# Kernel tuning notes

Measured on AMD Instinct MI355X. Metric: run time of the kernel, lower is better.

Reference implementation:

```python
import jax, jax.numpy as jnp
import numpy as np

B, T, D, H = 64, 1024, 256, 256

def setup_inputs() -> dict:
    key = jax.random.key(0)
    k1, k2, k3 = jax.random.split(key, 3)
    s = 1.0 / np.sqrt(H)
    return {
        "x": jax.random.normal(k1, (B, T, D), dtype=jnp.float32),
        "W_ih": jax.random.uniform(k2, (H, D), dtype=jnp.float32, minval=-s, maxval=s),
        "W_hh": jax.random.uniform(k3, (H, H), dtype=jnp.float32, minval=-s, maxval=s),
        "b_ih": jnp.zeros((H,), dtype=jnp.float32),
        "b_hh": jnp.zeros((H,), dtype=jnp.float32),
    }

def reference(x, W_ih, W_hh, b_ih, b_hh):
    # Precompute input projections for all timesteps at once (same math,
    # avoids T small GEMMs): [B, T, H]
    x_proj = jnp.einsum("btd,hd->bth", x, W_ih) + b_ih
    h0 = jnp.zeros((x.shape[0], W_hh.shape[0]), dtype=x.dtype)

    def step(h, xp_t):
        h_new = jnp.tanh(xp_t + h @ W_hh.T + b_hh)
        return h_new, h_new  # output of vanilla RNN cell is the new hidden state

    # scan over time: xp time-major [T, B, H]
    _, outs = jax.lax.scan(step, h0, jnp.swapaxes(x_proj, 0, 1))
    return jnp.swapaxes(outs, 0, 1)  # [B, T, H]
```

## Files before the change

### kernel.cpp

```cpp
#include <hip/hip_runtime.h>

#define BB 64
#define TT 1024
#define DD 256
#define HH 256
#define CH 8
#define NCH (TT / CH)

typedef float vf4 __attribute__((ext_vector_type(4)));
typedef float vf2 __attribute__((ext_vector_type(2)));
struct alignas(16) v2x2 { vf2 lo, hi; };

#define LD4(p) (*(const vf4*)(p))
#define LD2(p) (*(const vf2*)(p))
#define LDW(p) (*(const v2x2*)(p))

__device__ __forceinline__ float fast_tanh(float x) {
    float e = __expf(2.0f * x);
    return 1.0f - 2.0f / (e + 1.0f);
}

#define PKFMA(acc, aa, bb) acc = __builtin_elementwise_fma((aa), (bb), (acc))

#define DPPADD(dst, src, CTRL) {                                                   \
    int _di = __builtin_amdgcn_update_dpp(0, __float_as_int(src), CTRL, 0xF, 0xF, true); \
    dst = (src) + __int_as_float(_di); }

#define FMR(rr, bb, ss)                   \
    rr.x = fmaf((ss), (bb).x, rr.x);      \
    rr.y = fmaf((ss), (bb).y, rr.y);      \
    rr.z = fmaf((ss), (bb).z, rr.z);      \
    rr.w = fmaf((ss), (bb).w, rr.w)

#define BKb 32
#define LDP 132

__global__ __attribute__((amdgpu_flat_work_group_size(256, 256),
                          amdgpu_waves_per_eu(4, 4)))
void xproj_kernel(const float* __restrict__ x, const float* __restrict__ W_ih,
                  const float* __restrict__ b_ih, float* __restrict__ xp)
{
    __shared__ float As[BKb][LDP];
    __shared__ float Bs[BKb][LDP];

    const int tid = threadIdx.x;
    const int nb = blockIdx.x & 1;
    const int mb = blockIdx.x >> 1;
    const int m0 = mb * 128;
    const int n0 = nb * 128;

    const int sr = tid >> 3;
    const int sk = (tid & 7) * 4;

    const int tx = tid & 15;
    const int ty = tid >> 4;
    const int ma = ty * 4, mh = 64 + ty * 4;
    const int na = tx * 4, nh = 64 + tx * 4;

    vf4 ra0 = 0, ra1 = 0, ra2 = 0, ra3 = 0, ra4 = 0, ra5 = 0, ra6 = 0, ra7 = 0;
    vf4 rb0 = 0, rb1 = 0, rb2 = 0, rb3 = 0, rb4 = 0, rb5 = 0, rb6 = 0, rb7 = 0;

    for (int k0 = 0; k0 < DD; k0 += BKb) {
        #pragma unroll
        for (int g = 0; g < 4; ++g) {
            const int r = sr + g * 32;
            const vf4 v = LD4(x + (size_t)(m0 + r) * DD + k0 + sk);
            As[sk + 0][r] = v.x; As[sk + 1][r] = v.y;
            As[sk + 2][r] = v.z; As[sk + 3][r] = v.w;
        }
        #pragma unroll
        for (int g = 0; g < 4; ++g) {
            const int n = sr + g * 32;
            const vf4 v = LD4(W_ih + (size_t)(n0 + n) * DD + k0 + sk);
            Bs[sk + 0][n] = v.x; Bs[sk + 1][n] = v.y;
            Bs[sk + 2][n] = v.z; Bs[sk + 3][n] = v.w;
        }
        __syncthreads();

        #pragma unroll
        for (int kk = 0; kk < BKb; ++kk) {
            const vf4 alo = LD4(&As[kk][ma]);
            const vf4 ahi = LD4(&As[kk][mh]);
            const vf4 bl  = LD4(&Bs[kk][na]);
            const vf4 bh  = LD4(&Bs[kk][nh]);
            FMR(ra0, bl, alo.x); FMR(rb0, bh, alo.x);
            FMR(ra1, bl, alo.y); FMR(rb1, bh, alo.y);
            FMR(ra2, bl, alo.z); FMR(rb2, bh, alo.z);
            FMR(ra3, bl, alo.w); FMR(rb3, bh, alo.w);
            FMR(ra4, bl, ahi.x); FMR(rb4, bh, ahi.x);
            FMR(ra5, bl, ahi.y); FMR(rb5, bh, ahi.y);
            FMR(ra6, bl, ahi.z); FMR(rb6, bh, ahi.z);
            FMR(ra7, bl, ahi.w); FMR(rb7, bh, ahi.w);
        }
        __syncthreads();
    }

    const vf4 bia = LD4(b_ih + n0 + na);
    const vf4 bib = LD4(b_ih + n0 + nh);

    #define STORE_ROW(m, rA, rB)                                   \
        {                                                          \
            float* outp = xp + (size_t)(m0 + (m)) * HH + n0;       \
            *(vf4*)(outp + na) = rA + bia;                         \
            *(vf4*)(outp + nh) = rB + bib;                         \
        }
    STORE_ROW(ma + 0, ra0, rb0); STORE_ROW(ma + 1, ra1, rb1);
    STORE_ROW(ma + 2, ra2, rb2); STORE_ROW(ma + 3, ra3, rb3);
    STORE_ROW(mh + 0, ra4, rb4); STORE_ROW(mh + 1, ra5, rb5);
    STORE_ROW(mh + 2, ra6, rb6); STORE_ROW(mh + 3, ra7, rb7);
    #undef STORE_ROW
}

__global__ __attribute__((amdgpu_flat_work_group_size(1024, 1024),
                          amdgpu_waves_per_eu(4, 4)))
void rnn_kernel(const float* __restrict__ W_hh, const float* __restrict__ b_hh,
                const float* __restrict__ xpin, float* __restrict__ hout)
{
    const int tid = threadIdx.x;
    const int jg = tid >> 4;
    const int c  = tid & 15;
    const int j0 = jg * 4;
    const int jmine = j0 + (c & 3);
    const int b = blockIdx.x;

    __shared__ float hbuf[2][16 * 20];
    __shared__ float xchk[2][CH * HH];
    __shared__ float obuf[2][CH * HH];

    const float* wr0 = W_hh + (size_t)(j0 + 0) * HH + c * 16;
    const float* wr1 = W_hh + (size_t)(j0 + 1) * HH + c * 16;
    const float* wr2 = W_hh + (size_t)(j0 + 2) * HH + c * 16;
    const float* wr3 = W_hh + (size_t)(j0 + 3) * HH + c * 16;
    v2x2 w00 = LDW(wr0 + 0), w01 = LDW(wr0 + 4), w02 = LDW(wr0 + 8), w03 = LDW(wr0 + 12);
    v2x2 w10 = LDW(wr1 + 0), w11 = LDW(wr1 + 4), w12 = LDW(wr1 + 8), w13 = LDW(wr1 + 12);
    v2x2 w20 = LDW(wr2 + 0), w21 = LDW(wr2 + 4), w22 = LDW(wr2 + 8), w23 = LDW(wr2 + 12);
    v2x2 w30 = LDW(wr3 + 0), w31 = LDW(wr3 + 4), w32 = LDW(wr3 + 8), w33 = LDW(wr3 + 12);
    const float bias = b_hh[jmine];

    const float* xbase = xpin + (size_t)b * TT * HH;
    float*       obase = hout + (size_t)b * TT * HH;
    const int haddr = ((jmine >> 4) * 20) + (jmine & 15);

    vf2 r = LD2(xbase + tid * 2);
    if (tid < 320) hbuf[0][tid] = 0.0f;
    *(vf2*)&xchk[0][tid * 2] = r;
    r = LD2(xbase + CH * HH + tid * 2);
    __syncthreads();

    for (int ci = 0; ci < NCH; ++ci) {
        const int cb = ci & 1;

        #pragma unroll
        for (int s = 0; s < CH; ++s) {
            asm volatile("" : "+v"(w00.lo), "+v"(w00.hi), "+v"(w01.lo), "+v"(w01.hi),
                              "+v"(w02.lo), "+v"(w02.hi), "+v"(w03.lo), "+v"(w03.hi),
                              "+v"(w10.lo), "+v"(w10.hi), "+v"(w11.lo), "+v"(w11.hi),
                              "+v"(w12.lo), "+v"(w12.hi), "+v"(w13.lo), "+v"(w13.hi));
            asm volatile("" : "+v"(w20.lo), "+v"(w20.hi), "+v"(w21.lo), "+v"(w21.hi),
                              "+v"(w22.lo), "+v"(w22.hi), "+v"(w23.lo), "+v"(w23.hi),
                              "+v"(w30.lo), "+v"(w30.hi), "+v"(w31.lo), "+v"(w31.hi),
                              "+v"(w32.lo), "+v"(w32.hi), "+v"(w33.lo), "+v"(w33.hi));

            const float xpv = xchk[cb][s * HH + jmine];

            const float* hc = &hbuf[s & 1][c * 20];
            const v2x2 h0 = LDW(hc + 0), h1 = LDW(hc + 4),
                       h2 = LDW(hc + 8), h3 = LDW(hc + 12);

            vf2 a0 = {0.f, 0.f}, a1 = {0.f, 0.f}, a2 = {0.f, 0.f}, a3 = {0.f, 0.f};
            PKFMA(a0, w00.lo, h0.lo); PKFMA(a1, w10.lo, h0.lo);
            PKFMA(a2, w20.lo, h0.lo); PKFMA(a3, w30.lo, h0.lo);
            PKFMA(a0, w00.hi, h0.hi); PKFMA(a1, w10.hi, h0.hi);
            PKFMA(a2, w20.hi, h0.hi); PKFMA(a3, w30.hi, h0.hi);
            PKFMA(a0, w01.lo, h1.lo); PKFMA(a1, w11.lo, h1.lo);
            PKFMA(a2, w21.lo, h1.lo); PKFMA(a3, w31.lo, h1.lo);
            PKFMA(a0, w01.hi, h1.hi); PKFMA(a1, w11.hi, h1.hi);
            PKFMA(a2, w21.hi, h1.hi); PKFMA(a3, w31.hi, h1.hi);
            PKFMA(a0, w02.lo, h2.lo); PKFMA(a1, w12.lo, h2.lo);
            PKFMA(a2, w22.lo, h2.lo); PKFMA(a3, w32.lo, h2.lo);
            PKFMA(a0, w02.hi, h2.hi); PKFMA(a1, w12.hi, h2.hi);
            PKFMA(a2, w22.hi, h2.hi); PKFMA(a3, w32.hi, h2.hi);
            PKFMA(a0, w03.lo, h3.lo); PKFMA(a1, w13.lo, h3.lo);
            PKFMA(a2, w23.lo, h3.lo); PKFMA(a3, w33.lo, h3.lo);
            PKFMA(a0, w03.hi, h3.hi); PKFMA(a1, w13.hi, h3.hi);
            PKFMA(a2, w23.hi, h3.hi); PKFMA(a3, w33.hi, h3.hi);

            const float s0 = a0.x + a0.y, s1 = a1.x + a1.y,
                        s2 = a2.x + a2.y, s3 = a3.x + a3.y;

            float t0, t1, t2, t3, b0v, b1v, u0, u1, vfin;
            DPPADD(t0, s0, 0xB1); DPPADD(t1, s1, 0xB1);
            DPPADD(t2, s2, 0xB1); DPPADD(t3, s3, 0xB1);
            b0v = (c & 1) ? t1 : t0;
            b1v = (c & 1) ? t3 : t2;
            DPPADD(u0, b0v, 0x4E); DPPADD(u1, b1v, 0x4E);
            vfin = (c & 2) ? u1 : u0;
            DPPADD(vfin, vfin, 0x124);
            DPPADD(vfin, vfin, 0x128);

            if (s == CH - 1 && ci != NCH - 1) {
                *(vf2*)&xchk[cb ^ 1][tid * 2] = r;
            }

            const float hn = fast_tanh(vfin + xpv + bias);
            if (c < 4) {
                hbuf[1 - (s & 1)][haddr] = hn;
                obuf[cb][s * HH + jmine] = hn;
            }
            __syncthreads();
        }

        const vf2 ov = *(const vf2*)&obuf[cb][tid * 2];
        *(vf2*)(obase + (size_t)ci * CH * HH + tid * 2) = ov;
        if (ci + 2 < NCH) {
            r = LD2(xbase + (size_t)(ci + 2) * CH * HH + tid * 2);
        }
    }
}

extern "C" void kernel_launch(void* const* d_in, const int* in_sizes, int n_in,
                              void* d_out, int out_size, void* d_ws, size_t ws_size,
                              hipStream_t stream) {
    const float* x    = (const float*)d_in[0];
    const float* W_ih = (const float*)d_in[1];
    const float* W_hh = (const float*)d_in[2];
    const float* b_ih = (const float*)d_in[3];
    const float* b_hh = (const float*)d_in[4];
    float* out = (float*)d_out;

    const size_t xp_bytes = (size_t)BB * TT * HH * sizeof(float);
    float* xp = (ws_size >= xp_bytes) ? (float*)d_ws : out;

    xproj_kernel<<<dim3(512 * 2), dim3(256), 0, stream>>>(x, W_ih, b_ih, xp);
    rnn_kernel<<<dim3(BB), dim3(1024), 0, stream>>>(W_hh, b_hh, xp, out);
}
```

Baseline: 855.3 us.

## Halve RNN block to 512 threads with eight W_hh rows per thread

Each thread now keeps eight rows of W_hh in registers instead of four, so the recurrent kernel runs with 512 threads per block instead of 1024. The per-step DPP reduction gains one more select level, and the xp-chunk prefetch and output stores widen to vf4. Fewer waves should make each per-timestep __syncthreads cheaper. In exchange each wave carries roughly twice the register pressure and twice the FMA work per step, and the launch bounds drop to 2 waves per EU.

```diff
diff --git a/kernel.cpp b/kernel.cpp
--- a/kernel.cpp
+++ b/kernel.cpp
@@ -111,109 +111,147 @@
     #undef STORE_ROW
 }
 
-__global__ __attribute__((amdgpu_flat_work_group_size(1024, 1024),
-                          amdgpu_waves_per_eu(4, 4)))
+__global__ __attribute__((amdgpu_flat_work_group_size(512, 512),
+                          amdgpu_waves_per_eu(2, 2)))
 void rnn_kernel(const float* __restrict__ W_hh, const float* __restrict__ b_hh,
                 const float* __restrict__ xpin, float* __restrict__ hout)
 {
     const int tid = threadIdx.x;
     const int jg = tid >> 4;
     const int c  = tid & 15;
-    const int j0 = jg * 4;
-    const int jmine = j0 + (c & 3);
+    const int j0 = jg * 8;
+    const int jmine = j0 + (c & 7);
     const int b = blockIdx.x;
 
     __shared__ float hbuf[2][16 * 20];
     __shared__ float xchk[2][CH * HH];
     __shared__ float obuf[2][CH * HH];
 
-    const float* wr0 = W_hh + (size_t)(j0 + 0) * HH + c * 16;
-    const float* wr1 = W_hh + (size_t)(j0 + 1) * HH + c * 16;
-    const float* wr2 = W_hh + (size_t)(j0 + 2) * HH + c * 16;
-    const float* wr3 = W_hh + (size_t)(j0 + 3) * HH + c * 16;
-    v2x2 w00 = LDW(wr0 + 0), w01 = LDW(wr0 + 4), w02 = LDW(wr0 + 8), w03 = LDW(wr0 + 12);
-    v2x2 w10 = LDW(wr1 + 0), w11 = LDW(wr1 + 4), w12 = LDW(wr1 + 8), w13 = LDW(wr1 + 12);
-    v2x2 w20 = LDW(wr2 + 0), w21 = LDW(wr2 + 4), w22 = LDW(wr2 + 8), w23 = LDW(wr2 + 12);
-    v2x2 w30 = LDW(wr3 + 0), w31 = LDW(wr3 + 4), w32 = LDW(wr3 + 8), w33 = LDW(wr3 + 12);
+    v2x2 w[8][4];
+    #pragma unroll
+    for (int r = 0; r < 8; ++r) {
+        const float* wr = W_hh + (size_t)(j0 + r) * HH + c * 16;
+        w[r][0] = LDW(wr + 0);  w[r][1] = LDW(wr + 4);
+        w[r][2] = LDW(wr + 8);  w[r][3] = LDW(wr + 12);
+    }
     const float bias = b_hh[jmine];
 
     const float* xbase = xpin + (size_t)b * TT * HH;
     float*       obase = hout + (size_t)b * TT * HH;
     const int haddr = ((jmine >> 4) * 20) + (jmine & 15);
 
-    vf2 r = LD2(xbase + tid * 2);
+    vf4 rpf = LD4(xbase + tid * 4);
     if (tid < 320) hbuf[0][tid] = 0.0f;
-    *(vf2*)&xchk[0][tid * 2] = r;
-    r = LD2(xbase + CH * HH + tid * 2);
+    *(vf4*)&xchk[0][tid * 4] = rpf;
+    rpf = LD4(xbase + CH * HH + tid * 4);
     __syncthreads();
 
     for (int ci = 0; ci < NCH; ++ci) {
         const int cb = ci & 1;
 
+        asm volatile("" : "+v"(w[0][0].lo), "+v"(w[0][0].hi), "+v"(w[0][1].lo), "+v"(w[0][1].hi),
+                          "+v"(w[0][2].lo), "+v"(w[0][2].hi), "+v"(w[0][3].lo), "+v"(w[0][3].hi),
+                          "+v"(w[1][0].lo), "+v"(w[1][0].hi), "+v"(w[1][1].lo), "+v"(w[1][1].hi),
+                          "+v"(w[1][2].lo), "+v"(w[1][2].hi), "+v"(w[1][3].lo), "+v"(w[1][3].hi));
+        asm volatile("" : "+v"(w[2][0].lo), "+v"(w[2][0].hi), "+v"(w[2][1].lo), "+v"(w[2][1].hi),
+                          "+v"(w[2][2].lo), "+v"(w[2][2].hi), "+v"(w[2][3].lo), "+v"(w[2][3].hi),
+                          "+v"(w[3][0].lo), "+v"(w[3][0].hi), "+v"(w[3][1].lo), "+v"(w[3][1].hi),
+                          "+v"(w[3][2].lo), "+v"(w[3][2].hi), "+v"(w[3][3].lo), "+v"(w[3][3].hi));
+        asm volatile("" : "+v"(w[4][0].lo), "+v"(w[4][0].hi), "+v"(w[4][1].lo), "+v"(w[4][1].hi),
+                          "+v"(w[4][2].lo), "+v"(w[4][2].hi), "+v"(w[4][3].lo), "+v"(w[4][3].hi),
+                          "+v"(w[5][0].lo), "+v"(w[5][0].hi), "+v"(w[5][1].lo), "+v"(w[5][1].hi),
+                          "+v"(w[5][2].lo), "+v"(w[5][2].hi), "+v"(w[5][3].lo), "+v"(w[5][3].hi));
+        asm volatile("" : "+v"(w[6][0].lo), "+v"(w[6][0].hi), "+v"(w[6][1].lo), "+v"(w[6][1].hi),
+                          "+v"(w[6][2].lo), "+v"(w[6][2].hi), "+v"(w[6][3].lo), "+v"(w[6][3].hi),
+                          "+v"(w[7][0].lo), "+v"(w[7][0].hi), "+v"(w[7][1].lo), "+v"(w[7][1].hi),
+                          "+v"(w[7][2].lo), "+v"(w[7][2].hi), "+v"(w[7][3].lo), "+v"(w[7][3].hi));
+
+        const float* xc = &xchk[cb][0];
+        float*       ob = &obuf[cb][0];
+
         #pragma unroll
         for (int s = 0; s < CH; ++s) {
-            asm volatile("" : "+v"(w00.lo), "+v"(w00.hi), "+v"(w01.lo), "+v"(w01.hi),
-                              "+v"(w02.lo), "+v"(w02.hi), "+v"(w03.lo), "+v"(w03.hi),
-                              "+v"(w10.lo), "+v"(w10.hi), "+v"(w11.lo), "+v"(w11.hi),
-                              "+v"(w12.lo), "+v"(w12.hi), "+v"(w13.lo), "+v"(w13.hi));
-            asm volatile("" : "+v"(w20.lo), "+v"(w20.hi), "+v"(w21.lo), "+v"(w21.hi),
-                              "+v"(w22.lo), "+v"(w22.hi), "+v"(w23.lo), "+v"(w23.hi),
-                              "+v"(w30.lo), "+v"(w30.hi), "+v"(w31.lo), "+v"(w31.hi),
-                              "+v"(w32.lo), "+v"(w32.hi), "+v"(w33.lo), "+v"(w33.hi));
-
-            const float xpv = xchk[cb][s * HH + jmine];
+            const float xpb = xc[s * HH + jmine] + bias;
 
             const float* hc = &hbuf[s & 1][c * 20];
             const v2x2 h0 = LDW(hc + 0), h1 = LDW(hc + 4),
                        h2 = LDW(hc + 8), h3 = LDW(hc + 12);
 
             vf2 a0 = {0.f, 0.f}, a1 = {0.f, 0.f}, a2 = {0.f, 0.f}, a3 = {0.f, 0.f};
-            PKFMA(a0, w00.lo, h0.lo); PKFMA(a1, w10.lo, h0.lo);
-            PKFMA(a2, w20.lo, h0.lo); PKFMA(a3, w30.lo, h0.lo);
-            PKFMA(a0, w00.hi, h0.hi); PKFMA(a1, w10.hi, h0.hi);
-            PKFMA(a2, w20.hi, h0.hi); PKFMA(a3, w30.hi, h0.hi);
-            PKFMA(a0, w01.lo, h1.lo); PKFMA(a1, w11.lo, h1.lo);
-            PKFMA(a2, w21.lo, h1.lo); PKFMA(a3, w31.lo, h1.lo);
-            PKFMA(a0, w01.hi, h1.hi); PKFMA(a1, w11.hi, h1.hi);
-            PKFMA(a2, w21.hi, h1.hi); PKFMA(a3, w31.hi, h1.hi);
-            PKFMA(a0, w02.lo, h2.lo); PKFMA(a1, w12.lo, h2.lo);
-            PKFMA(a2, w22.lo, h2.lo); PKFMA(a3, w32.lo, h2.lo);
-            PKFMA(a0, w02.hi, h2.hi); PKFMA(a1, w12.hi, h2.hi);
-            PKFMA(a2, w22.hi, h2.hi); PKFMA(a3, w32.hi, h2.hi);
-            PKFMA(a0, w03.lo, h3.lo); PKFMA(a1, w13.lo, h3.lo);
-            PKFMA(a2, w23.lo, h3.lo); PKFMA(a3, w33.lo, h3.lo);
-            PKFMA(a0, w03.hi, h3.hi); PKFMA(a1, w13.hi, h3.hi);
-            PKFMA(a2, w23.hi, h3.hi); PKFMA(a3, w33.hi, h3.hi);
+            vf2 a4 = {0.f, 0.f}, a5 = {0.f, 0.f}, a6 = {0.f, 0.f}, a7 = {0.f, 0.f};
+            PKFMA(a0, w[0][0].lo, h0.lo); PKFMA(a0, w[0][0].hi, h0.hi);
+            PKFMA(a0, w[0][1].lo, h1.lo); PKFMA(a0, w[0][1].hi, h1.hi);
+            PKFMA(a0, w[0][2].lo, h2.lo); PKFMA(a0, w[0][2].hi, h2.hi);
+            PKFMA(a0, w[0][3].lo, h3.lo); PKFMA(a0, w[0][3].hi, h3.hi);
+            PKFMA(a1, w[1][0].lo, h0.lo); PKFMA(a1, w[1][0].hi, h0.hi);
+            PKFMA(a1, w[1][1].lo, h1.lo); PKFMA(a1, w[1][1].hi, h1.hi);
+            PKFMA(a1, w[1][2].lo, h2.lo); PKFMA(a1, w[1][2].hi, h2.hi);
+            PKFMA(a1, w[1][3].lo, h3.lo); PKFMA(a1, w[1][3].hi, h3.hi);
+            PKFMA(a2, w[2][0].lo, h0.lo); PKFMA(a2, w[2][0].hi, h0.hi);
+            PKFMA(a2, w[2][1].lo, h1.lo); PKFMA(a2, w[2][1].hi, h1.hi);
+            PKFMA(a2, w[2][2].lo, h2.lo); PKFMA(a2, w[2][2].hi, h2.hi);
+            PKFMA(a2, w[2][3].lo, h3.lo); PKFMA(a2, w[2][3].hi, h3.hi);
+            PKFMA(a3, w[3][0].lo, h0.lo); PKFMA(a3, w[3][0].hi, h0.hi);
+            PKFMA(a3, w[3][1].lo, h1.lo); PKFMA(a3, w[3][1].hi, h1.hi);
+            PKFMA(a3, w[3][2].lo, h2.lo); PKFMA(a3, w[3][2].hi, h2.hi);
+            PKFMA(a3, w[3][3].lo, h3.lo); PKFMA(a3, w[3][3].hi, h3.hi);
+            PKFMA(a4, w[4][0].lo, h0.lo); PKFMA(a4, w[4][0].hi, h0.hi);
+            PKFMA(a4, w[4][1].lo, h1.lo); PKFMA(a4, w[4][1].hi, h1.hi);
+            PKFMA(a4, w[4][2].lo, h2.lo); PKFMA(a4, w[4][2].hi, h2.hi);
+            PKFMA(a4, w[4][3].lo, h3.lo); PKFMA(a4, w[4][3].hi, h3.hi);
+            PKFMA(a5, w[5][0].lo, h0.lo); PKFMA(a5, w[5][0].hi, h0.hi);
+            PKFMA(a5, w[5][1].lo, h1.lo); PKFMA(a5, w[5][1].hi, h1.hi);
+            PKFMA(a5, w[5][2].lo, h2.lo); PKFMA(a5, w[5][2].hi, h2.hi);
+            PKFMA(a5, w[5][3].lo, h3.lo); PKFMA(a5, w[5][3].hi, h3.hi);
+            PKFMA(a6, w[6][0].lo, h0.lo); PKFMA(a6, w[6][0].hi, h0.hi);
+            PKFMA(a6, w[6][1].lo, h1.lo); PKFMA(a6, w[6][1].hi, h1.hi);
+            PKFMA(a6, w[6][2].lo, h2.lo); PKFMA(a6, w[6][2].hi, h2.hi);
+            PKFMA(a6, w[6][3].lo, h3.lo); PKFMA(a6, w[6][3].hi, h3.hi);
+            PKFMA(a7, w[7][0].lo, h0.lo); PKFMA(a7, w[7][0].hi, h0.hi);
+            PKFMA(a7, w[7][1].lo, h1.lo); PKFMA(a7, w[7][1].hi, h1.hi);
+            PKFMA(a7, w[7][2].lo, h2.lo); PKFMA(a7, w[7][2].hi, h2.hi);
+            PKFMA(a7, w[7][3].lo, h3.lo); PKFMA(a7, w[7][3].hi, h3.hi);
 
             const float s0 = a0.x + a0.y, s1 = a1.x + a1.y,
-                        s2 = a2.x + a2.y, s3 = a3.x + a3.y;
-
-            float t0, t1, t2, t3, b0v, b1v, u0, u1, vfin;
+                        s2 = a2.x + a2.y, s3 = a3.x + a3.y,
+                        s4 = a4.x + a4.y, s5 = a5.x + a5.y,
+                        s6 = a6.x + a6.y, s7 = a7.x + a7.y;
+
+            float t0, t1, t2, t3, t4, t5, t6, t7;
             DPPADD(t0, s0, 0xB1); DPPADD(t1, s1, 0xB1);
             DPPADD(t2, s2, 0xB1); DPPADD(t3, s3, 0xB1);
-            b0v = (c & 1) ? t1 : t0;
-            b1v = (c & 1) ? t3 : t2;
-            DPPADD(u0, b0v, 0x4E); DPPADD(u1, b1v, 0x4E);
-            vfin = (c & 2) ? u1 : u0;
-            DPPADD(vfin, vfin, 0x124);
+            DPPADD(t4, s4, 0xB1); DPPADD(t5, s5, 0xB1);
+            DPPADD(t6, s6, 0xB1); DPPADD(t7, s7, 0xB1);
+            const float p0 = (c & 1) ? t1 : t0;
+            const float p1 = (c & 1) ? t3 : t2;
+            const float p2 = (c & 1) ? t5 : t4;
+            const float p3 = (c & 1) ? t7 : t6;
+            float u0, u1, u2, u3;
+            DPPADD(u0, p0, 0x4E); DPPADD(u1, p1, 0x4E);
+            DPPADD(u2, p2, 0x4E); DPPADD(u3, p3, 0x4E);
+            const float v0 = (c & 2) ? u1 : u0;
+            const float v1 = (c & 2) ? u3 : u2;
+            float q0, q1;
+            DPPADD(q0, v0, 0x124); DPPADD(q1, v1, 0x124);
+            float vfin = (c & 4) ? q1 : q0;
             DPPADD(vfin, vfin, 0x128);
 
             if (s == CH - 1 && ci != NCH - 1) {
-                *(vf2*)&xchk[cb ^ 1][tid * 2] = r;
+                *(vf4*)&xchk[cb ^ 1][tid * 4] = rpf;
             }
 
-            const float hn = fast_tanh(vfin + xpv + bias);
-            if (c < 4) {
+            const float hn = fast_tanh(vfin + xpb);
+            if (c < 8) {
                 hbuf[1 - (s & 1)][haddr] = hn;
-                obuf[cb][s * HH + jmine] = hn;
+                ob[s * HH + jmine] = hn;
             }
             __syncthreads();
         }
 
-        const vf2 ov = *(const vf2*)&obuf[cb][tid * 2];
-        *(vf2*)(obase + (size_t)ci * CH * HH + tid * 2) = ov;
+        const vf4 ov = *(const vf4*)&obuf[cb][tid * 4];
+        *(vf4*)(obase + (size_t)ci * CH * HH + tid * 4) = ov;
         if (ci + 2 < NCH) {
-            r = LD2(xbase + (size_t)(ci + 2) * CH * HH + tid * 2);
+            rpf = LD4(xbase + (size_t)(ci + 2) * CH * HH + tid * 4);
         }
     }
 }
@@ -232,5 +270,5 @@
     float* xp = (ws_size >= xp_bytes) ? (float*)d_ws : out;
 
     xproj_kernel<<<dim3(512 * 2), dim3(256), 0, stream>>>(x, W_ih, b_ih, xp);
-    rnn_kernel<<<dim3(BB), dim3(1024), 0, stream>>>(W_hh, b_hh, xp, out);
-}
+    rnn_kernel<<<dim3(BB), dim3(512), 0, stream>>>(W_hh, b_hh, xp, out);
+}
```

Measured after the change: 783.7 us. -8.4%, faster.

## Shrink RNN block to 256 threads with 16 rows of W_hh per thread

Applied to the files above, without the earlier changes.

The recurrent kernel now uses 256 threads per batch instead of 1024. Each thread keeps 16 rows × 16 columns of W_hh in registers (256 floats) and does a 16-lane DPP butterfly reduction that ends with one output per lane. Fewer waves make each per-step __syncthreads cheaper, and the FMAs are now written as inline packed-FMA asm. In exchange, each step does four times as much serial compute per thread, register pressure is very high with a risk of spills, and the inline asm stops the compiler from rescheduling those instructions.

```diff
diff --git a/kernel.cpp b/kernel.cpp
--- a/kernel.cpp
+++ b/kernel.cpp
@@ -12,7 +12,6 @@
 struct alignas(16) v2x2 { vf2 lo, hi; };
 
 #define LD4(p) (*(const vf4*)(p))
-#define LD2(p) (*(const vf2*)(p))
 #define LDW(p) (*(const v2x2*)(p))
 
 __device__ __forceinline__ float fast_tanh(float x) {
@@ -20,7 +19,10 @@
     return 1.0f - 2.0f / (e + 1.0f);
 }
 
-#define PKFMA(acc, aa, bb) acc = __builtin_elementwise_fma((aa), (bb), (acc))
+#define APKMUL(acc, ww, hh) \
+    asm("v_pk_mul_f32 %0, %1, %2" : "=v"(acc) : "v"(ww), "v"(hh))
+#define APKFMA(acc, ww, hh) \
+    asm("v_pk_fma_f32 %0, %1, %2, %0" : "+v"(acc) : "v"(ww), "v"(hh))
 
 #define DPPADD(dst, src, CTRL) {                                                   \
     int _di = __builtin_amdgcn_update_dpp(0, __float_as_int(src), CTRL, 0xF, 0xF, true); \
@@ -111,109 +113,127 @@
     #undef STORE_ROW
 }
 
-__global__ __attribute__((amdgpu_flat_work_group_size(1024, 1024),
-                          amdgpu_waves_per_eu(4, 4)))
+__global__ __attribute__((amdgpu_flat_work_group_size(256, 256),
+                          amdgpu_waves_per_eu(1, 1)))
 void rnn_kernel(const float* __restrict__ W_hh, const float* __restrict__ b_hh,
                 const float* __restrict__ xpin, float* __restrict__ hout)
 {
     const int tid = threadIdx.x;
     const int jg = tid >> 4;
     const int c  = tid & 15;
-    const int j0 = jg * 4;
-    const int jmine = j0 + (c & 3);
+    const int j0 = jg * 16;
+    const int jmine = j0 + c;
     const int b = blockIdx.x;
 
     __shared__ float hbuf[2][16 * 20];
     __shared__ float xchk[2][CH * HH];
     __shared__ float obuf[2][CH * HH];
 
-    const float* wr0 = W_hh + (size_t)(j0 + 0) * HH + c * 16;
-    const float* wr1 = W_hh + (size_t)(j0 + 1) * HH + c * 16;
-    const float* wr2 = W_hh + (size_t)(j0 + 2) * HH + c * 16;
-    const float* wr3 = W_hh + (size_t)(j0 + 3) * HH + c * 16;
-    v2x2 w00 = LDW(wr0 + 0), w01 = LDW(wr0 + 4), w02 = LDW(wr0 + 8), w03 = LDW(wr0 + 12);
-    v2x2 w10 = LDW(wr1 + 0), w11 = LDW(wr1 + 4), w12 = LDW(wr1 + 8), w13 = LDW(wr1 + 12);
-    v2x2 w20 = LDW(wr2 + 0), w21 = LDW(wr2 + 4), w22 = LDW(wr2 + 8), w23 = LDW(wr2 + 12);
-    v2x2 w30 = LDW(wr3 + 0), w31 = LDW(wr3 + 4), w32 = LDW(wr3 + 8), w33 = LDW(wr3 + 12);
+    v2x2 w[16][4];
+    #pragma unroll
+    for (int r = 0; r < 16; ++r) {
+        const float* wr = W_hh + (size_t)(j0 + r) * HH + c * 16;
+        w[r][0] = LDW(wr + 0);  w[r][1] = LDW(wr + 4);
+        w[r][2] = LDW(wr + 8);  w[r][3] = LDW(wr + 12);
+    }
     const float bias = b_hh[jmine];
+
+    #define PINROW2(r0, r1) \
+        asm volatile("" : "+v"(w[r0][0].lo), "+v"(w[r0][0].hi), "+v"(w[r0][1].lo), "+v"(w[r0][1].hi), \
+                          "+v"(w[r0][2].lo), "+v"(w[r0][2].hi), "+v"(w[r0][3].lo), "+v"(w[r0][3].hi), \
+                          "+v"(w[r1][0].lo), "+v"(w[r1][0].hi), "+v"(w[r1][1].lo), "+v"(w[r1][1].hi), \
+                          "+v"(w[r1][2].lo), "+v"(w[r1][2].hi), "+v"(w[r1][3].lo), "+v"(w[r1][3].hi))
+    PINROW2(0, 1);  PINROW2(2, 3);  PINROW2(4, 5);  PINROW2(6, 7);
+    PINROW2(8, 9);  PINROW2(10, 11); PINROW2(12, 13); PINROW2(14, 15);
+    #undef PINROW2
 
     const float* xbase = xpin + (size_t)b * TT * HH;
     float*       obase = hout + (size_t)b * TT * HH;
-    const int haddr = ((jmine >> 4) * 20) + (jmine & 15);
-
-    vf2 r = LD2(xbase + tid * 2);
-    if (tid < 320) hbuf[0][tid] = 0.0f;
-    *(vf2*)&xchk[0][tid * 2] = r;
-    r = LD2(xbase + CH * HH + tid * 2);
+    const int haddr = jg * 20 + c;
+
+    vf4 rpf0 = LD4(xbase + tid * 8);
+    vf4 rpf1 = LD4(xbase + tid * 8 + 4);
+    hbuf[0][tid] = 0.0f;
+    if (tid < 64) hbuf[0][256 + tid] = 0.0f;
+    *(vf4*)&xchk[0][tid * 8]     = rpf0;
+    *(vf4*)&xchk[0][tid * 8 + 4] = rpf1;
+    rpf0 = LD4(xbase + CH * HH + tid * 8);
+    rpf1 = LD4(xbase + CH * HH + tid * 8 + 4);
     __syncthreads();
 
     for (int ci = 0; ci < NCH; ++ci) {
         const int cb = ci & 1;
 
-        #pragma unroll
+        const float* xc = &xchk[cb][0];
+        float*       ob = &obuf[cb][0];
+
+        #pragma unroll 2
         for (int s = 0; s < CH; ++s) {
-            asm volatile("" : "+v"(w00.lo), "+v"(w00.hi), "+v"(w01.lo), "+v"(w01.hi),
-                              "+v"(w02.lo), "+v"(w02.hi), "+v"(w03.lo), "+v"(w03.hi),
-                              "+v"(w10.lo), "+v"(w10.hi), "+v"(w11.lo), "+v"(w11.hi),
-                              "+v"(w12.lo), "+v"(w12.hi), "+v"(w13.lo), "+v"(w13.hi));
-            asm volatile("" : "+v"(w20.lo), "+v"(w20.hi), "+v"(w21.lo), "+v"(w21.hi),
-                              "+v"(w22.lo), "+v"(w22.hi), "+v"(w23.lo), "+v"(w23.hi),
-                              "+v"(w30.lo), "+v"(w30.hi), "+v"(w31.lo), "+v"(w31.hi),
-                              "+v"(w32.lo), "+v"(w32.hi), "+v"(w33.lo), "+v"(w33.hi));
-
-            const float xpv = xchk[cb][s * HH + jmine];
+            const float xpb = xc[s * HH + jmine] + bias;
 
             const float* hc = &hbuf[s & 1][c * 20];
             const v2x2 h0 = LDW(hc + 0), h1 = LDW(hc + 4),
                        h2 = LDW(hc + 8), h3 = LDW(hc + 12);
 
-            vf2 a0 = {0.f, 0.f}, a1 = {0.f, 0.f}, a2 = {0.f, 0.f}, a3 = {0.f, 0.f};
-            PKFMA(a0, w00.lo, h0.lo); PKFMA(a1, w10.lo, h0.lo);
-            PKFMA(a2, w20.lo, h0.lo); PKFMA(a3, w30.lo, h0.lo);
-            PKFMA(a0, w00.hi, h0.hi); PKFMA(a1, w10.hi, h0.hi);
-            PKFMA(a2, w20.hi, h0.hi); PKFMA(a3, w30.hi, h0.hi);
-            PKFMA(a0, w01.lo, h1.lo); PKFMA(a1, w11.lo, h1.lo);
-            PKFMA(a2, w21.lo, h1.lo); PKFMA(a3, w31.lo, h1.lo);
-            PKFMA(a0, w01.hi, h1.hi); PKFMA(a1, w11.hi, h1.hi);
-            PKFMA(a2, w21.hi, h1.hi); PKFMA(a3, w31.hi, h1.hi);
-            PKFMA(a0, w02.lo, h2.lo); PKFMA(a1, w12.lo, h2.lo);
-            PKFMA(a2, w22.lo, h2.lo); PKFMA(a3, w32.lo, h2.lo);
-            PKFMA(a0, w02.hi, h2.hi); PKFMA(a1, w12.hi, h2.hi);
-            PKFMA(a2, w22.hi, h2.hi); PKFMA(a3, w32.hi, h2.hi);
-            PKFMA(a0, w03.lo, h3.lo); PKFMA(a1, w13.lo, h3.lo);
-            PKFMA(a2, w23.lo, h3.lo); PKFMA(a3, w33.lo, h3.lo);
-            PKFMA(a0, w03.hi, h3.hi); PKFMA(a1, w13.hi, h3.hi);
-            PKFMA(a2, w23.hi, h3.hi); PKFMA(a3, w33.hi, h3.hi);
-
-            const float s0 = a0.x + a0.y, s1 = a1.x + a1.y,
-                        s2 = a2.x + a2.y, s3 = a3.x + a3.y;
-
-            float t0, t1, t2, t3, b0v, b1v, u0, u1, vfin;
-            DPPADD(t0, s0, 0xB1); DPPADD(t1, s1, 0xB1);
-            DPPADD(t2, s2, 0xB1); DPPADD(t3, s3, 0xB1);
-            b0v = (c & 1) ? t1 : t0;
-            b1v = (c & 1) ? t3 : t2;
-            DPPADD(u0, b0v, 0x4E); DPPADD(u1, b1v, 0x4E);
-            vfin = (c & 2) ? u1 : u0;
-            DPPADD(vfin, vfin, 0x124);
-            DPPADD(vfin, vfin, 0x128);
+            vf2 aa[16];
+            #pragma unroll
+            for (int r = 0; r < 16; ++r) {
+                APKMUL(aa[r], w[r][0].lo, h0.lo);
+                APKFMA(aa[r], w[r][0].hi, h0.hi);
+                APKFMA(aa[r], w[r][1].lo, h1.lo);
+                APKFMA(aa[r], w[r][1].hi, h1.hi);
+                APKFMA(aa[r], w[r][2].lo, h2.lo);
+                APKFMA(aa[r], w[r][2].hi, h2.hi);
+                APKFMA(aa[r], w[r][3].lo, h3.lo);
+                APKFMA(aa[r], w[r][3].hi, h3.hi);
+            }
+
+            float sv[16];
+            #pragma unroll
+            for (int i = 0; i < 16; ++i) sv[i] = aa[i].x + aa[i].y;
+
+            float tv[16];
+            #pragma unroll
+            for (int i = 0; i < 16; ++i) { DPPADD(tv[i], sv[i], 0xB1); }
+            float pv[8];
+            #pragma unroll
+            for (int i = 0; i < 8; ++i) pv[i] = (c & 1) ? tv[2 * i + 1] : tv[2 * i];
+            float uv[8];
+            #pragma unroll
+            for (int i = 0; i < 8; ++i) { DPPADD(uv[i], pv[i], 0x4E); }
+            float vv[4];
+            #pragma unroll
+            for (int i = 0; i < 4; ++i) vv[i] = (c & 2) ? uv[2 * i + 1] : uv[2 * i];
+            float qv[4];
+            #pragma unroll
+            for (int i = 0; i < 4; ++i) { DPPADD(qv[i], vv[i], 0x124); }
+            float rv[2];
+            #pragma unroll
+            for (int i = 0; i < 2; ++i) rv[i] = (c & 4) ? qv[2 * i + 1] : qv[2 * i];
+            float ev[2];
+            #pragma unroll
+            for (int i = 0; i < 2; ++i) { DPPADD(ev[i], rv[i], 0x128); }
+            const float vfin = (c & 8) ? ev[1] : ev[0];
 
             if (s == CH - 1 && ci != NCH - 1) {
-                *(vf2*)&xchk[cb ^ 1][tid * 2] = r;
+                *(vf4*)&xchk[cb ^ 1][tid * 8]     = rpf0;
+                *(vf4*)&xchk[cb ^ 1][tid * 8 + 4] = rpf1;
             }
 
-            const float hn = fast_tanh(vfin + xpv + bias);
-            if (c < 4) {
-                hbuf[1 - (s & 1)][haddr] = hn;
-                obuf[cb][s * HH + jmine] = hn;
-            }
+            const float hn = fast_tanh(vfin + xpb);
+            hbuf[1 - (s & 1)][haddr] = hn;
+            ob[s * HH + jmine] = hn;
             __syncthreads();
         }
 
-        const vf2 ov = *(const vf2*)&obuf[cb][tid * 2];
-        *(vf2*)(obase + (size_t)ci * CH * HH + tid * 2) = ov;
+        const vf4 ov0 = *(const vf4*)&obuf[cb][tid * 8];
+        const vf4 ov1 = *(const vf4*)&obuf[cb][tid * 8 + 4];
+        float* op = obase + (size_t)ci * CH * HH + tid * 8;
+        *(vf4*)(op)     = ov0;
+        *(vf4*)(op + 4) = ov1;
         if (ci + 2 < NCH) {
-            r = LD2(xbase + (size_t)(ci + 2) * CH * HH + tid * 2);
+            rpf0 = LD4(xbase + (size_t)(ci + 2) * CH * HH + tid * 8);
+            rpf1 = LD4(xbase + (size_t)(ci + 2) * CH * HH + tid * 8 + 4);
         }
     }
 }
@@ -232,5 +252,5 @@
     float* xp = (ws_size >= xp_bytes) ? (float*)d_ws : out;
 
     xproj_kernel<<<dim3(512 * 2), dim3(256), 0, stream>>>(x, W_ih, b_ih, xp);
-    rnn_kernel<<<dim3(BB), dim3(1024), 0, stream>>>(W_hh, b_hh, xp, out);
-}
+    rnn_kernel<<<dim3(BB), dim3(256), 0, stream>>>(W_hh, b_hh, xp, out);
+}
```

Measured after the change: 2.678 ms. +213.1%, slower.

## Use split-bf16 MFMA for the recurrent matvec instead of packed FP32 FMAs

Applied to the files above, without the earlier changes.

The recurrent step now runs on 16x16x32 bf16 MFMA. W_hh and h are each split into high and low bf16 parts, and three products are summed to keep close to fp32 accuracy. The block drops from 1024 to 512 threads, with each wave owning 32 output columns. The DPP cross-lane reduction is gone, and obuf is now single-buffered behind an extra barrier. In exchange, the 16-row MFMA tile is mostly wasted because only one batch row is real, each step costs 48 dependent MFMAs, and only 16 lanes per wave do the tanh epilogue.

```diff
diff --git a/kernel.cpp b/kernel.cpp
--- a/kernel.cpp
+++ b/kernel.cpp
@@ -8,23 +8,20 @@
 #define NCH (TT / CH)
 
 typedef float vf4 __attribute__((ext_vector_type(4)));
-typedef float vf2 __attribute__((ext_vector_type(2)));
-struct alignas(16) v2x2 { vf2 lo, hi; };
+typedef float f32x4 __attribute__((ext_vector_type(4)));
+typedef short bf16x8 __attribute__((ext_vector_type(8)));
 
 #define LD4(p) (*(const vf4*)(p))
-#define LD2(p) (*(const vf2*)(p))
-#define LDW(p) (*(const v2x2*)(p))
 
 __device__ __forceinline__ float fast_tanh(float x) {
     float e = __expf(2.0f * x);
     return 1.0f - 2.0f / (e + 1.0f);
 }
 
-#define PKFMA(acc, aa, bb) acc = __builtin_elementwise_fma((aa), (bb), (acc))
-
-#define DPPADD(dst, src, CTRL) {                                                   \
-    int _di = __builtin_amdgcn_update_dpp(0, __float_as_int(src), CTRL, 0xF, 0xF, true); \
-    dst = (src) + __int_as_float(_di); }
+__device__ __forceinline__ unsigned bf16rne(float f) {
+    unsigned u = __float_as_uint(f);
+    return (u + 0x7FFFu + ((u >> 16) & 1u)) >> 16;
+}
 
 #define FMR(rr, bb, ss)                   \
     rr.x = fmaf((ss), (bb).x, rr.x);      \
@@ -111,110 +108,113 @@
     #undef STORE_ROW
 }
 
-__global__ __attribute__((amdgpu_flat_work_group_size(1024, 1024),
-                          amdgpu_waves_per_eu(4, 4)))
+#define HSTR 264
+
+__global__ __attribute__((amdgpu_flat_work_group_size(512, 512),
+                          amdgpu_waves_per_eu(2, 2)))
 void rnn_kernel(const float* __restrict__ W_hh, const float* __restrict__ b_hh,
                 const float* __restrict__ xpin, float* __restrict__ hout)
 {
-    const int tid = threadIdx.x;
-    const int jg = tid >> 4;
-    const int c  = tid & 15;
-    const int j0 = jg * 4;
-    const int jmine = j0 + (c & 3);
-    const int b = blockIdx.x;
-
-    __shared__ float hbuf[2][16 * 20];
-    __shared__ float xchk[2][CH * HH];
-    __shared__ float obuf[2][CH * HH];
-
-    const float* wr0 = W_hh + (size_t)(j0 + 0) * HH + c * 16;
-    const float* wr1 = W_hh + (size_t)(j0 + 1) * HH + c * 16;
-    const float* wr2 = W_hh + (size_t)(j0 + 2) * HH + c * 16;
-    const float* wr3 = W_hh + (size_t)(j0 + 3) * HH + c * 16;
-    v2x2 w00 = LDW(wr0 + 0), w01 = LDW(wr0 + 4), w02 = LDW(wr0 + 8), w03 = LDW(wr0 + 12);
-    v2x2 w10 = LDW(wr1 + 0), w11 = LDW(wr1 + 4), w12 = LDW(wr1 + 8), w13 = LDW(wr1 + 12);
-    v2x2 w20 = LDW(wr2 + 0), w21 = LDW(wr2 + 4), w22 = LDW(wr2 + 8), w23 = LDW(wr2 + 12);
-    v2x2 w30 = LDW(wr3 + 0), w31 = LDW(wr3 + 4), w32 = LDW(wr3 + 8), w33 = LDW(wr3 + 12);
-    const float bias = b_hh[jmine];
+    const int tid  = threadIdx.x;
+    const int lane = tid & 63;
+    const int wid  = tid >> 6;
+    const int rrow = lane & 15;
+    const int kgrp = lane >> 4;
+    const int b    = blockIdx.x;
+
+    __shared__ __align__(16) short Hs[4][16 * HSTR];
+    __shared__ __align__(16) float xchk[2][CH * HH];
+    __shared__ __align__(16) float obuf[CH * HH];
+
+    bf16x8 wf[2][2][8];
+    #pragma unroll
+    for (int t = 0; t < 2; ++t) {
+        const int n = (wid * 2 + t) * 16 + rrow;
+        #pragma unroll
+        for (int kk = 0; kk < 8; ++kk) {
+            const int k0 = kk * 32 + kgrp * 8;
+            const float* wp = W_hh + (size_t)n * HH + k0;
+            bf16x8 s1, s2;
+            #pragma unroll
+            for (int j = 0; j < 8; ++j) {
+                const float f = wp[j];
+                const unsigned r1 = bf16rne(f);
+                const float f1 = __uint_as_float(r1 << 16);
+                const unsigned r2 = bf16rne(f - f1);
+                s1[j] = (short)r1;
+                s2[j] = (short)r2;
+            }
+            wf[t][0][kk] = s1;
+            wf[t][1][kk] = s2;
+        }
+    }
+    const float bias0 = b_hh[wid * 32 + rrow];
+    const float bias1 = b_hh[wid * 32 + 16 + rrow];
 
     const float* xbase = xpin + (size_t)b * TT * HH;
     float*       obase = hout + (size_t)b * TT * HH;
-    const int haddr = ((jmine >> 4) * 20) + (jmine & 15);
-
-    vf2 r = LD2(xbase + tid * 2);
-    if (tid < 320) hbuf[0][tid] = 0.0f;
-    *(vf2*)&xchk[0][tid * 2] = r;
-    r = LD2(xbase + CH * HH + tid * 2);
+
+    vf4 rpf = LD4(xbase + tid * 4);
+    for (int i = tid; i < 4 * 16 * HSTR / 2; i += 512) ((int*)Hs)[i] = 0;
+    *(vf4*)&xchk[0][tid * 4] = rpf;
+    rpf = LD4(xbase + CH * HH + tid * 4);
     __syncthreads();
 
     for (int ci = 0; ci < NCH; ++ci) {
         const int cb = ci & 1;
-
-        #pragma unroll
+        const float* xc = &xchk[cb][0];
+
+        #pragma unroll 2
         for (int s = 0; s < CH; ++s) {
-            asm volatile("" : "+v"(w00.lo), "+v"(w00.hi), "+v"(w01.lo), "+v"(w01.hi),
-                              "+v"(w02.lo), "+v"(w02.hi), "+v"(w03.lo), "+v"(w03.hi),
-                              "+v"(w10.lo), "+v"(w10.hi), "+v"(w11.lo), "+v"(w11.hi),
-                              "+v"(w12.lo), "+v"(w12.hi), "+v"(w13.lo), "+v"(w13.hi));
-            asm volatile("" : "+v"(w20.lo), "+v"(w20.hi), "+v"(w21.lo), "+v"(w21.hi),
-                              "+v"(w22.lo), "+v"(w22.hi), "+v"(w23.lo), "+v"(w23.hi),
-                              "+v"(w30.lo), "+v"(w30.hi), "+v"(w31.lo), "+v"(w31.hi),
-                              "+v"(w32.lo), "+v"(w32.hi), "+v"(w33.lo), "+v"(w33.hi));
-
-            const float xpv = xchk[cb][s * HH + jmine];
-
-            const float* hc = &hbuf[s & 1][c * 20];
-            const v2x2 h0 = LDW(hc + 0), h1 = LDW(hc + 4),
-                       h2 = LDW(hc + 8), h3 = LDW(hc + 12);
-
-            vf2 a0 = {0.f, 0.f}, a1 = {0.f, 0.f}, a2 = {0.f, 0.f}, a3 = {0.f, 0.f};
-            PKFMA(a0, w00.lo, h0.lo); PKFMA(a1, w10.lo, h0.lo);
-            PKFMA(a2, w20.lo, h0.lo); PKFMA(a3, w30.lo, h0.lo);
-            PKFMA(a0, w00.hi, h0.hi); PKFMA(a1, w10.hi, h0.hi);
-            PKFMA(a2, w20.hi, h0.hi); PKFMA(a3, w30.hi, h0.hi);
-            PKFMA(a0, w01.lo, h1.lo); PKFMA(a1, w11.lo, h1.lo);
-            PKFMA(a2, w21.lo, h1.lo); PKFMA(a3, w31.lo, h1.lo);
-            PKFMA(a0, w01.hi, h1.hi); PKFMA(a1, w11.hi, h1.hi);
-            PKFMA(a2, w21.hi, h1.hi); PKFMA(a3, w31.hi, h1.hi);
-            PKFMA(a0, w02.lo, h2.lo); PKFMA(a1, w12.lo, h2.lo);
-            PKFMA(a2, w22.lo, h2.lo); PKFMA(a3, w32.lo, h2.lo);
-            PKFMA(a0, w02.hi, h2.hi); PKFMA(a1, w12.hi, h2.hi);
-            PKFMA(a2, w22.hi, h2.hi); PKFMA(a3, w32.hi, h2.hi);
-            PKFMA(a0, w03.lo, h3.lo); PKFMA(a1, w13.lo, h3.lo);
-            PKFMA(a2, w23.lo, h3.lo); PKFMA(a3, w33.lo, h3.lo);
-            PKFMA(a0, w03.hi, h3.hi); PKFMA(a1, w13.hi, h3.hi);
-            PKFMA(a2, w23.hi, h3.hi); PKFMA(a3, w33.hi, h3.hi);
-
-            const float s0 = a0.x + a0.y, s1 = a1.x + a1.y,
-                        s2 = a2.x + a2.y, s3 = a3.x + a3.y;
-
-            float t0, t1, t2, t3, b0v, b1v, u0, u1, vfin;
-            DPPADD(t0, s0, 0xB1); DPPADD(t1, s1, 0xB1);
-            DPPADD(t2, s2, 0xB1); DPPADD(t3, s3, 0xB1);
-            b0v = (c & 1) ? t1 : t0;
-            b1v = (c & 1) ? t3 : t2;
-            DPPADD(u0, b0v, 0x4E); DPPADD(u1, b1v, 0x4E);
-            vfin = (c & 2) ? u1 : u0;
-            DPPADD(vfin, vfin, 0x124);
-            DPPADD(vfin, vfin, 0x128);
+            const short* A1 = &Hs[(s & 1) * 2 + 0][0];
+            const short* A2 = &Hs[(s & 1) * 2 + 1][0];
+            short* N1 = &Hs[((s + 1) & 1) * 2 + 0][0];
+            short* N2 = &Hs[((s + 1) & 1) * 2 + 1][0];
+
+            f32x4 ac0 = {0.f, 0.f, 0.f, 0.f};
+            f32x4 ac1 = {0.f, 0.f, 0.f, 0.f};
+
+            #pragma unroll
+            for (int kk = 0; kk < 8; ++kk) {
+                const int k0 = kk * 32 + kgrp * 8;
+                const bf16x8 a1 = *(const bf16x8*)&A1[rrow * HSTR + k0];
+                const bf16x8 a2 = *(const bf16x8*)&A2[rrow * HSTR + k0];
+                ac0 = __builtin_amdgcn_mfma_f32_16x16x32_bf16(a1, wf[0][0][kk], ac0, 0, 0, 0);
+                ac1 = __builtin_amdgcn_mfma_f32_16x16x32_bf16(a1, wf[1][0][kk], ac1, 0, 0, 0);
+                ac0 = __builtin_amdgcn_mfma_f32_16x16x32_bf16(a2, wf[0][0][kk], ac0, 0, 0, 0);
+                ac1 = __builtin_amdgcn_mfma_f32_16x16x32_bf16(a2, wf[1][0][kk], ac1, 0, 0, 0);
+                ac0 = __builtin_amdgcn_mfma_f32_16x16x32_bf16(a1, wf[0][1][kk], ac0, 0, 0, 0);
+                ac1 = __builtin_amdgcn_mfma_f32_16x16x32_bf16(a1, wf[1][1][kk], ac1, 0, 0, 0);
+            }
 
             if (s == CH - 1 && ci != NCH - 1) {
-                *(vf2*)&xchk[cb ^ 1][tid * 2] = r;
-            }
-
-            const float hn = fast_tanh(vfin + xpv + bias);
-            if (c < 4) {
-                hbuf[1 - (s & 1)][haddr] = hn;
-                obuf[cb][s * HH + jmine] = hn;
+                *(vf4*)&xchk[cb ^ 1][tid * 4] = rpf;
+            }
+
+            if (lane < 16) {
+                #pragma unroll
+                for (int t = 0; t < 2; ++t) {
+                    const int n = (wid * 2 + t) * 16 + lane;
+                    const float acc = t ? ac1[0] : ac0[0];
+                    const float v = acc + xc[s * HH + n] + (t ? bias1 : bias0);
+                    const float hn = fast_tanh(v);
+                    const unsigned r1 = bf16rne(hn);
+                    const float h1f = __uint_as_float(r1 << 16);
+                    const unsigned r2 = bf16rne(hn - h1f);
+                    N1[n] = (short)r1;
+                    N2[n] = (short)r2;
+                    obuf[s * HH + n] = hn;
+                }
             }
             __syncthreads();
         }
 
-        const vf2 ov = *(const vf2*)&obuf[cb][tid * 2];
-        *(vf2*)(obase + (size_t)ci * CH * HH + tid * 2) = ov;
+        const vf4 ov = *(const vf4*)&obuf[tid * 4];
+        *(vf4*)(obase + (size_t)ci * CH * HH + tid * 4) = ov;
         if (ci + 2 < NCH) {
-            r = LD2(xbase + (size_t)(ci + 2) * CH * HH + tid * 2);
-        }
+            rpf = LD4(xbase + (size_t)(ci + 2) * CH * HH + tid * 4);
+        }
+        __syncthreads();
     }
 }
 
@@ -232,5 +232,5 @@
     float* xp = (ws_size >= xp_bytes) ? (float*)d_ws : out;
 
     xproj_kernel<<<dim3(512 * 2), dim3(256), 0, stream>>>(x, W_ih, b_ih, xp);
-    rnn_kernel<<<dim3(BB), dim3(1024), 0, stream>>>(W_hh, b_hh, xp, out);
-}
+    rnn_kernel<<<dim3(BB), dim3(512), 0, stream>>>(W_hh, b_hh, xp, out);
+}
```

After: 1.236 ms. +44.5%, slower.
